# Optimization experiments

Measured on AMD Instinct MI355X. Metric: run time of the kernel, lower is better.

Reference implementation:

```python
import jax, jax.numpy as jnp
import numpy as np

NUM_FEATURES = 128
NUM_FILTERS = 128

def setup_inputs() -> dict:
    key = jax.random.key(0)
    k1, k2, k3, k4, k5 = jax.random.split(key, 5)
    B, N, F = 4, 2048, NUM_FEATURES
    x = jax.random.normal(k1, (B, N, F), dtype=jnp.float32)
    A = jax.random.normal(k2, (B, N, N), dtype=jnp.float32)
    # Conv1D(num_filters, kernel_size=1, use_bias=False) == per-node linear F -> filters
    W = jax.random.normal(k3, (F, NUM_FILTERS), dtype=jnp.float32) * (1.0 / np.sqrt(F))
    # self.a: Conv1D(1, kernel_size=1) with bias == linear filters -> 1 (shared for x_i and x_j)
    a_w = jax.random.normal(k4, (NUM_FILTERS, 1), dtype=jnp.float32) * (1.0 / np.sqrt(NUM_FILTERS))
    a_b = jax.random.normal(k5, (1,), dtype=jnp.float32) * 0.01
    bias = jnp.zeros((NUM_FILTERS,), dtype=jnp.float32)
    return {"x": x, "A": A, "W": W, "a_w": a_w, "a_b": a_b, "bias": bias}

def reference(x, A, W, a_w, a_b, bias):
    # project features: [B,N,F] @ [F,Ff] -> [B,N,Ff]
    h = jnp.einsum('bnf,fg->bng', x, W)
    # shared attention projection (x_i and x_j use the same layer): [B,N,1]
    s = jnp.einsum('bng,go->bno', h, a_w) + a_b
    # additive scores s_i + s_j^T -> [B,N,N]
    e = s + jnp.swapaxes(s, 1, 2)
    e = jnp.where(e >= 0, e, 0.2 * e)  # LeakyReLU(0.2)
    attn = jax.nn.softmax(e + A, axis=-1)
    out = jnp.einsum('bij,bjg->big', attn, h) + bias
    return out
```

## Files before the change

### kernel.cpp

```cpp
#include <hip/hip_runtime.h>
#include <hip/hip_bf16.h>
#include <stdint.h>

#define BB 4
#define NN 2048
#define FF 128

typedef __attribute__((ext_vector_type(8))) short bf16x8;
typedef __attribute__((ext_vector_type(4))) float f32x4;

__device__ inline unsigned pk_bf16(float a, float b) {
    union { float f; unsigned u; } x, y;
    x.f = a; y.f = b;
    unsigned xu = x.u + (0x7fffu + ((x.u >> 16) & 1u));
    unsigned yu = y.u + (0x7fffu + ((y.u >> 16) & 1u));
    return (xu >> 16) | (yu & 0xffff0000u);
}

#define XT_P 136
#define WT_P 136

__global__ __launch_bounds__(256) void k1_proj(
    const float* __restrict__ x, const float* __restrict__ W,
    const float* __restrict__ a_w, const float* __restrict__ a_b,
    uint16_t* __restrict__ Ht, float* __restrict__ s_out)
{
    __shared__ uint16_t xt[16 * XT_P];
    __shared__ uint16_t Wt[128 * WT_P];
    __shared__ float sredw[4 * 16];

    const int t = threadIdx.x;
    const int w = t >> 6, l = t & 63;
    const int m16 = l & 15, q = l >> 4;
    const int b = blockIdx.x >> 7;
    const int n0 = (blockIdx.x & 127) << 4;

    const int c4 = (t & 31) * 4, kh = (t >> 5) * 16;
    float4 wr0[8], wr1[8];
    #pragma unroll
    for (int kk = 0; kk < 8; ++kk) {
        const int k = kh + 2 * kk;
        wr0[kk] = *(const float4*)(W + (size_t)k * 128 + c4);
        wr1[kk] = *(const float4*)(W + (size_t)(k + 1) * 128 + c4);
    }
    {
        const int row = t >> 4, c0 = (t & 15) * 8;
        const float* xr = x + ((size_t)(b * NN + n0 + row)) * FF + c0;
        const float4 v0 = *(const float4*)xr;
        const float4 v1 = *(const float4*)(xr + 4);
        unsigned* dst = (unsigned*)(xt + row * XT_P + c0);
        dst[0] = pk_bf16(v0.x, v0.y); dst[1] = pk_bf16(v0.z, v0.w);
        dst[2] = pk_bf16(v1.x, v1.y); dst[3] = pk_bf16(v1.z, v1.w);
    }
    #pragma unroll
    for (int kk = 0; kk < 8; ++kk) {
        const int k = kh + 2 * kk;
        *(unsigned*)(Wt + (c4 + 0) * WT_P + k) = pk_bf16(wr0[kk].x, wr1[kk].x);
        *(unsigned*)(Wt + (c4 + 1) * WT_P + k) = pk_bf16(wr0[kk].y, wr1[kk].y);
        *(unsigned*)(Wt + (c4 + 2) * WT_P + k) = pk_bf16(wr0[kk].z, wr1[kk].z);
        *(unsigned*)(Wt + (c4 + 3) * WT_P + k) = pk_bf16(wr0[kk].w, wr1[kk].w);
    }
    const int g0 = (2 * w) * 16 + m16, g1 = (2 * w + 1) * 16 + m16;
    const float aw0 = a_w[g0], aw1 = a_w[g1];
    __syncthreads();

    f32x4 acc0 = {}, acc1 = {};
    bf16x8 af[4];
    #pragma unroll
    for (int dk = 0; dk < 4; ++dk)
        af[dk] = *(const bf16x8*)(xt + m16 * XT_P + dk * 32 + q * 8);
    #pragma unroll
    for (int dk = 0; dk < 4; ++dk) {
        bf16x8 b0 = *(const bf16x8*)(Wt + g0 * WT_P + dk * 32 + q * 8);
        bf16x8 b1 = *(const bf16x8*)(Wt + g1 * WT_P + dk * 32 + q * 8);
        acc0 = __builtin_amdgcn_mfma_f32_16x16x32_bf16(af[dk], b0, acc0, 0, 0, 0);
        acc1 = __builtin_amdgcn_mfma_f32_16x16x32_bf16(af[dk], b1, acc1, 0, 0, 0);
    }

    float sp[4];
    #pragma unroll
    for (int r = 0; r < 4; ++r) sp[r] = acc0[r] * aw0 + acc1[r] * aw1;
    #pragma unroll
    for (int off = 1; off < 16; off <<= 1)
        #pragma unroll
        for (int r = 0; r < 4; ++r) sp[r] += __shfl_xor(sp[r], off, 64);
    if (m16 == 0) {
        #pragma unroll
        for (int r = 0; r < 4; ++r) sredw[w * 16 + q * 4 + r] = sp[r];
    }
    {
        uint2 o0 = { pk_bf16(acc0[0], acc0[1]), pk_bf16(acc0[2], acc0[3]) };
        uint2 o1 = { pk_bf16(acc1[0], acc1[1]), pk_bf16(acc1[2], acc1[3]) };
        *(uint2*)(Ht + ((size_t)(b * 128 + g0)) * NN + n0 + q * 4) = o0;
        *(uint2*)(Ht + ((size_t)(b * 128 + g1)) * NN + n0 + q * 4) = o1;
    }
    __syncthreads();
    if (t < 16)
        s_out[b * NN + n0 + t] = sredw[t] + sredw[16 + t] + sredw[32 + t] + sredw[48 + t] + a_b[0];
}

#define JS 8
#define IRND 8

__global__ __launch_bounds__(512, 3) void k2_attn(
    const float* __restrict__ A, const uint16_t* __restrict__ Ht,
    const float* __restrict__ s, uint16_t* __restrict__ po,
    float* __restrict__ prs)
{
    __shared__ float Opw[8][16 * 68];
    __shared__ float rsw[4][16];

    const int t = threadIdx.x;
    const int w = t >> 6, l = t & 63;
    const int m16 = l & 15, q = l >> 4;
    const int gh = w & 1, jh = w >> 1;

    const int bx = blockIdx.x;
    const int js = bx & 7;
    const int is = (bx >> 3) & 15;
    const int b  = bx >> 7;
    const int j0 = js * 256;
    const int ibase = is * 128;

    const float* sb = s + b * NN;
    const float* Ab = A + (size_t)b * NN * NN;
    const uint16_t* Hb = Ht + (size_t)b * FF * NN;

    const int jcb = j0 + jh * 64;
    const int jq0 = jcb + q * 8;
    const int jq1 = jcb + 32 + q * 8;

    float4 sj0 = *(const float4*)(sb + jq0);
    float4 sj1 = *(const float4*)(sb + jq0 + 4);
    float4 sj2 = *(const float4*)(sb + jq1);
    float4 sj3 = *(const float4*)(sb + jq1 + 4);

    bf16x8 hf[4][2];
    #pragma unroll
    for (int gt = 0; gt < 4; ++gt) {
        const uint16_t* hp = Hb + (size_t)(gh * 64 + gt * 16 + m16) * NN;
        hf[gt][0] = *(const bf16x8*)(hp + jq0);
        hf[gt][1] = *(const bf16x8*)(hp + jq1);
    }

    const float* Ar = Ab + (size_t)(ibase + m16) * NN;
    float4 a0 = *(const float4*)(Ar + jq0);
    float4 a1 = *(const float4*)(Ar + jq0 + 4);
    float4 a2 = *(const float4*)(Ar + jq1);
    float4 a3 = *(const float4*)(Ar + jq1 + 4);
    float si = sb[ibase + m16];

    const size_t slice = (size_t)(js * BB + b);

    for (int r = 0; r < IRND; ++r) {
        const int i0r = ibase + r * 16;
        const int i0n = ibase + ((r + 1) & (IRND - 1)) * 16;

        const float* An = Ab + (size_t)(i0n + m16) * NN;
        float4 n0 = *(const float4*)(An + jq0);
        float4 n1 = *(const float4*)(An + jq0 + 4);
        float4 n2 = *(const float4*)(An + jq1);
        float4 n3 = *(const float4*)(An + jq1 + 4);
        const float sin_ = sb[i0n + m16];

        const float svv[16] = {sj0.x,sj0.y,sj0.z,sj0.w, sj1.x,sj1.y,sj1.z,sj1.w,
                               sj2.x,sj2.y,sj2.z,sj2.w, sj3.x,sj3.y,sj3.z,sj3.w};
        const float avv[16] = {a0.x,a0.y,a0.z,a0.w, a1.x,a1.y,a1.z,a1.w,
                               a2.x,a2.y,a2.z,a2.w, a3.x,a3.y,a3.z,a3.w};
        float pv[16]; float rs = 0.f;
        #pragma unroll
        for (int j = 0; j < 16; ++j) {
            float e = si + svv[j];
            e = fmaxf(e, 0.2f * e);
            pv[j] = __expf(e + avv[j]);
            rs += pv[j];
        }
        union { unsigned u[4]; bf16x8 v; } fa0, fa1;
        #pragma unroll
        for (int j = 0; j < 4; ++j) {
            fa0.u[j] = pk_bf16(pv[2 * j], pv[2 * j + 1]);
            fa1.u[j] = pk_bf16(pv[8 + 2 * j], pv[9 + 2 * j]);
        }

        f32x4 acc[4];
        #pragma unroll
        for (int gt = 0; gt < 4; ++gt) {
            f32x4 z = {0.f, 0.f, 0.f, 0.f};
            z = __builtin_amdgcn_mfma_f32_16x16x32_bf16(fa0.v, hf[gt][0], z, 0, 0, 0);
            acc[gt] = __builtin_amdgcn_mfma_f32_16x16x32_bf16(fa1.v, hf[gt][1], z, 0, 0, 0);
        }

        rs += __shfl_xor(rs, 16, 64);
        rs += __shfl_xor(rs, 32, 64);
        if (gh == 0 && q == 0) rsw[jh][m16] = rs;

        #pragma unroll
        for (int gt = 0; gt < 4; ++gt)
            #pragma unroll
            for (int rr = 0; rr < 4; ++rr)
                Opw[w][(q * 4 + rr) * 68 + gt * 16 + m16] = acc[gt][rr];
        asm volatile("s_waitcnt lgkmcnt(0)\n\ts_barrier" ::: "memory");

        {
            const int row = t >> 5;
            const int c4 = (t & 31) * 4;
            const int gh2 = c4 >> 6;
            const int cc = c4 & 63;
            float4 v = {0.f, 0.f, 0.f, 0.f};
            #pragma unroll
            for (int jh2 = 0; jh2 < 4; ++jh2) {
                float4 u = *(const float4*)&Opw[jh2 * 2 + gh2][row * 68 + cc];
                v.x += u.x; v.y += u.y; v.z += u.z; v.w += u.w;
            }
            unsigned* op = (unsigned*)(po + ((slice * NN + i0r + row) * FF + c4));
            op[0] = pk_bf16(v.x, v.y);
            op[1] = pk_bf16(v.z, v.w);
            if (t < 16)
                prs[slice * NN + i0r + t] = rsw[0][t] + rsw[1][t] + rsw[2][t] + rsw[3][t];
        }
        asm volatile("s_waitcnt lgkmcnt(0)\n\ts_barrier" ::: "memory");

        a0 = n0; a1 = n1; a2 = n2; a3 = n3; si = sin_;
    }
}

__global__ __launch_bounds__(256) void k3_red(
    const uint16_t* __restrict__ po, const float* __restrict__ prs,
    const float* __restrict__ bias, float* __restrict__ out)
{
    const int idx = blockIdx.x * 256 + threadIdx.x;
    const int g4 = (idx & 31) * 4;
    const int i = (idx >> 5) & (NN - 1);
    const int b = idx >> 16;

    float v0 = 0.f, v1 = 0.f, v2 = 0.f, v3 = 0.f, rsum = 0.f;
    #pragma unroll
    for (int js = 0; js < JS; ++js) {
        const size_t base = (size_t)(js * BB + b) * NN + i;
        uint2 u = *(const uint2*)(po + base * FF + g4);
        union { unsigned u; float f; } c0, c1, c2, c3;
        c0.u = u.x << 16; c1.u = u.x & 0xffff0000u;
        c2.u = u.y << 16; c3.u = u.y & 0xffff0000u;
        v0 += c0.f; v1 += c1.f; v2 += c2.f; v3 += c3.f;
        rsum += prs[base];
    }
    const float inv = 1.0f / rsum;
    float4 bv = *(const float4*)(bias + g4);
    float4 o = { v0 * inv + bv.x, v1 * inv + bv.y, v2 * inv + bv.z, v3 * inv + bv.w };
    *(float4*)(out + ((size_t)b * NN + i) * FF + g4) = o;
}

extern "C" void kernel_launch(void* const* d_in, const int* in_sizes, int n_in,
                              void* d_out, int out_size, void* d_ws, size_t ws_size,
                              hipStream_t stream) {
    const float* x    = (const float*)d_in[0];
    const float* A    = (const float*)d_in[1];
    const float* W    = (const float*)d_in[2];
    const float* a_w  = (const float*)d_in[3];
    const float* a_b  = (const float*)d_in[4];
    const float* bias = (const float*)d_in[5];
    float* out = (float*)d_out;

    char* ws = (char*)d_ws;
    uint16_t* Ht = (uint16_t*)ws;
    float* s = (float*)(ws + 2 * 1024 * 1024);
    uint16_t* po = (uint16_t*)(ws + 2 * 1024 * 1024 + 65536);
    float* prs = (float*)(ws + 2 * 1024 * 1024 + 65536 + (size_t)JS * BB * NN * FF * 2);

    k1_proj<<<BB * (NN / 16), 256, 0, stream>>>(x, W, a_w, a_b, Ht, s);
    k2_attn<<<JS * 16 * BB, 512, 0, stream>>>(A, Ht, s, po, prs);
    k3_red<<<(BB * NN * 32) / 256, 256, 0, stream>>>(po, prs, bias, out);
}
```

Baseline: 128.5 us.

## Fuse projection, attention and reduction into one cooperative kernel with grid syncs

Replaces the three separate launches with a single cooperative kernel of 256 blocks that runs projection, attention and the final reduction as phases separated by grid-wide syncs. Block work is re-partitioned so each block handles 32 nodes in projection and 256 query rows in attention, with a two-deep prefetch of A rows. Shared memory is a union of the phase layouts. This removes inter-kernel launch gaps and tail effects but adds grid barrier cost, reduces the number of blocks in the attention phase, and lowers occupancy to two blocks per CU.

```diff
diff --git a/kernel.cpp b/kernel.cpp
--- a/kernel.cpp
+++ b/kernel.cpp
@@ -1,10 +1,14 @@
 #include <hip/hip_runtime.h>
 #include <hip/hip_bf16.h>
+#include <hip/hip_cooperative_groups.h>
 #include <stdint.h>
+
+namespace cg = cooperative_groups;
 
 #define BB 4
 #define NN 2048
 #define FF 128
+#define JS 8
 
 typedef __attribute__((ext_vector_type(8))) short bf16x8;
 typedef __attribute__((ext_vector_type(4))) float f32x4;
@@ -20,234 +24,249 @@
 #define XT_P 136
 #define WT_P 136
 
-__global__ __launch_bounds__(256) void k1_proj(
-    const float* __restrict__ x, const float* __restrict__ W,
-    const float* __restrict__ a_w, const float* __restrict__ a_b,
-    uint16_t* __restrict__ Ht, float* __restrict__ s_out)
+struct SmemP1 {
+    uint16_t xt[32 * XT_P];
+    uint16_t Wt[128 * WT_P];
+    float sredw[2][64];
+};
+struct SmemP2 {
+    float Opw[8][16 * 68];
+    float rsw[4][16];
+};
+union Smem { SmemP1 p1; SmemP2 p2; };
+
+__global__ __launch_bounds__(512, 2) void fused_gat(
+    const float* __restrict__ x, const float* __restrict__ A,
+    const float* __restrict__ W, const float* __restrict__ a_w,
+    const float* __restrict__ a_b, const float* __restrict__ bias,
+    uint16_t* __restrict__ Ht, float* __restrict__ s,
+    uint16_t* __restrict__ po, float* __restrict__ prs,
+    float* __restrict__ out)
 {
-    __shared__ uint16_t xt[16 * XT_P];
-    __shared__ uint16_t Wt[128 * WT_P];
-    __shared__ float sredw[4 * 16];
+    __shared__ Smem sm;
+    cg::grid_group grid = cg::this_grid();
 
     const int t = threadIdx.x;
     const int w = t >> 6, l = t & 63;
     const int m16 = l & 15, q = l >> 4;
-    const int b = blockIdx.x >> 7;
-    const int n0 = (blockIdx.x & 127) << 4;
-
-    const int c4 = (t & 31) * 4, kh = (t >> 5) * 16;
-    float4 wr0[8], wr1[8];
-    #pragma unroll
-    for (int kk = 0; kk < 8; ++kk) {
-        const int k = kh + 2 * kk;
-        wr0[kk] = *(const float4*)(W + (size_t)k * 128 + c4);
-        wr1[kk] = *(const float4*)(W + (size_t)(k + 1) * 128 + c4);
-    }
+    const int bx = blockIdx.x;
+
     {
-        const int row = t >> 4, c0 = (t & 15) * 8;
-        const float* xr = x + ((size_t)(b * NN + n0 + row)) * FF + c0;
+        const int b = bx >> 6;
+        const int n0 = (bx & 63) << 5;
+
+        const int c4 = (t & 31) * 4, kseg = (t >> 5) * 8;
+        float4 wr[8];
+        #pragma unroll
+        for (int kk = 0; kk < 8; ++kk)
+            wr[kk] = *(const float4*)(W + (size_t)(kseg + kk) * 128 + c4);
+
+        const int xrow = t >> 4, xc0 = (t & 15) * 8;
+        const float* xr = x + ((size_t)(b * NN + n0 + xrow)) * FF + xc0;
         const float4 v0 = *(const float4*)xr;
         const float4 v1 = *(const float4*)(xr + 4);
-        unsigned* dst = (unsigned*)(xt + row * XT_P + c0);
-        dst[0] = pk_bf16(v0.x, v0.y); dst[1] = pk_bf16(v0.z, v0.w);
-        dst[2] = pk_bf16(v1.x, v1.y); dst[3] = pk_bf16(v1.z, v1.w);
+        {
+            unsigned* dst = (unsigned*)(sm.p1.xt + xrow * XT_P + xc0);
+            dst[0] = pk_bf16(v0.x, v0.y); dst[1] = pk_bf16(v0.z, v0.w);
+            dst[2] = pk_bf16(v1.x, v1.y); dst[3] = pk_bf16(v1.z, v1.w);
+        }
+        #pragma unroll
+        for (int i = 0; i < 4; ++i) {
+            unsigned* wd = (unsigned*)(sm.p1.Wt + (c4 + i) * WT_P + kseg);
+            wd[0] = pk_bf16(((const float*)&wr[0])[i], ((const float*)&wr[1])[i]);
+            wd[1] = pk_bf16(((const float*)&wr[2])[i], ((const float*)&wr[3])[i]);
+            wd[2] = pk_bf16(((const float*)&wr[4])[i], ((const float*)&wr[5])[i]);
+            wd[3] = pk_bf16(((const float*)&wr[6])[i], ((const float*)&wr[7])[i]);
+        }
+        const int rg = w >> 2, ws2 = w & 3;
+        const int g0 = (2 * ws2) * 16 + m16, g1 = (2 * ws2 + 1) * 16 + m16;
+        const float aw0 = a_w[g0], aw1 = a_w[g1];
+        __syncthreads();
+
+        f32x4 acc0 = {}, acc1 = {};
+        #pragma unroll
+        for (int dk = 0; dk < 4; ++dk) {
+            bf16x8 af = *(const bf16x8*)(sm.p1.xt + (rg * 16 + m16) * XT_P + dk * 32 + q * 8);
+            bf16x8 b0 = *(const bf16x8*)(sm.p1.Wt + g0 * WT_P + dk * 32 + q * 8);
+            bf16x8 b1 = *(const bf16x8*)(sm.p1.Wt + g1 * WT_P + dk * 32 + q * 8);
+            acc0 = __builtin_amdgcn_mfma_f32_16x16x32_bf16(af, b0, acc0, 0, 0, 0);
+            acc1 = __builtin_amdgcn_mfma_f32_16x16x32_bf16(af, b1, acc1, 0, 0, 0);
+        }
+        float sp[4];
+        #pragma unroll
+        for (int r = 0; r < 4; ++r) sp[r] = acc0[r] * aw0 + acc1[r] * aw1;
+        #pragma unroll
+        for (int off = 1; off < 16; off <<= 1)
+            #pragma unroll
+            for (int r = 0; r < 4; ++r) sp[r] += __shfl_xor(sp[r], off, 64);
+        if (m16 == 0) {
+            #pragma unroll
+            for (int r = 0; r < 4; ++r) sm.p1.sredw[rg][ws2 * 16 + q * 4 + r] = sp[r];
+        }
+        {
+            uint2 o0 = { pk_bf16(acc0[0], acc0[1]), pk_bf16(acc0[2], acc0[3]) };
+            uint2 o1 = { pk_bf16(acc1[0], acc1[1]), pk_bf16(acc1[2], acc1[3]) };
+            const int nb = n0 + rg * 16 + q * 4;
+            *(uint2*)(Ht + ((size_t)(b * FF + g0)) * NN + nb) = o0;
+            *(uint2*)(Ht + ((size_t)(b * FF + g1)) * NN + nb) = o1;
+        }
+        __syncthreads();
+        if (t < 32) {
+            const int rg2 = t >> 4, row = t & 15;
+            s[b * NN + n0 + rg2 * 16 + row] =
+                sm.p1.sredw[rg2][row] + sm.p1.sredw[rg2][16 + row] +
+                sm.p1.sredw[rg2][32 + row] + sm.p1.sredw[rg2][48 + row] + a_b[0];
+        }
     }
-    #pragma unroll
-    for (int kk = 0; kk < 8; ++kk) {
-        const int k = kh + 2 * kk;
-        *(unsigned*)(Wt + (c4 + 0) * WT_P + k) = pk_bf16(wr0[kk].x, wr1[kk].x);
-        *(unsigned*)(Wt + (c4 + 1) * WT_P + k) = pk_bf16(wr0[kk].y, wr1[kk].y);
-        *(unsigned*)(Wt + (c4 + 2) * WT_P + k) = pk_bf16(wr0[kk].z, wr1[kk].z);
-        *(unsigned*)(Wt + (c4 + 3) * WT_P + k) = pk_bf16(wr0[kk].w, wr1[kk].w);
+
+    __threadfence();
+    grid.sync();
+
+    {
+        const int gh = w & 1, jh = w >> 1;
+        const int js = bx & 7;
+        const int is = (bx >> 3) & 7;
+        const int b  = bx >> 6;
+        const int j0 = js * 256;
+        const int ibase = is * 256;
+
+        const float* sb = s + b * NN;
+        const float* Ab = A + (size_t)b * NN * NN;
+        const uint16_t* Hb = Ht + (size_t)b * FF * NN;
+
+        const int jcb = j0 + jh * 64;
+        const int jq0 = jcb + q * 8;
+        const int jq1 = jcb + 32 + q * 8;
+
+        float4 sj0 = *(const float4*)(sb + jq0);
+        float4 sj1 = *(const float4*)(sb + jq0 + 4);
+        float4 sj2 = *(const float4*)(sb + jq1);
+        float4 sj3 = *(const float4*)(sb + jq1 + 4);
+
+        bf16x8 hf[4][2];
+        #pragma unroll
+        for (int gt = 0; gt < 4; ++gt) {
+            const uint16_t* hp = Hb + (size_t)(gh * 64 + gt * 16 + m16) * NN;
+            hf[gt][0] = *(const bf16x8*)(hp + jq0);
+            hf[gt][1] = *(const bf16x8*)(hp + jq1);
+        }
+
+        const float* ArP = Ab + (size_t)(ibase + m16) * NN;
+        float4 p0 = *(const float4*)(ArP + jq0);
+        float4 p1 = *(const float4*)(ArP + jq0 + 4);
+        float4 p2 = *(const float4*)(ArP + jq1);
+        float4 p3 = *(const float4*)(ArP + jq1 + 4);
+        float siP = sb[ibase + m16];
+        const float* ArQ = Ab + (size_t)(ibase + 16 + m16) * NN;
+        float4 q0 = *(const float4*)(ArQ + jq0);
+        float4 q1 = *(const float4*)(ArQ + jq0 + 4);
+        float4 q2 = *(const float4*)(ArQ + jq1);
+        float4 q3 = *(const float4*)(ArQ + jq1 + 4);
+        float siQ = sb[ibase + 16 + m16];
+
+        const size_t slice = (size_t)(js * BB + b);
+
+        for (int r = 0; r < 16; ++r) {
+            const int i0r = ibase + r * 16;
+            const int i0n = ibase + ((r + 2) & 15) * 16;
+
+            const float* An = Ab + (size_t)(i0n + m16) * NN;
+            float4 n0_ = *(const float4*)(An + jq0);
+            float4 n1_ = *(const float4*)(An + jq0 + 4);
+            float4 n2_ = *(const float4*)(An + jq1);
+            float4 n3_ = *(const float4*)(An + jq1 + 4);
+            const float siN = sb[i0n + m16];
+
+            const float svv[16] = {sj0.x,sj0.y,sj0.z,sj0.w, sj1.x,sj1.y,sj1.z,sj1.w,
+                                   sj2.x,sj2.y,sj2.z,sj2.w, sj3.x,sj3.y,sj3.z,sj3.w};
+            const float avv[16] = {p0.x,p0.y,p0.z,p0.w, p1.x,p1.y,p1.z,p1.w,
+                                   p2.x,p2.y,p2.z,p2.w, p3.x,p3.y,p3.z,p3.w};
+            float pv[16]; float rs = 0.f;
+            #pragma unroll
+            for (int j = 0; j < 16; ++j) {
+                float e = siP + svv[j];
+                e = fmaxf(e, 0.2f * e);
+                pv[j] = __expf(e + avv[j]);
+                rs += pv[j];
+            }
+            union { unsigned u[4]; bf16x8 v; } fa0, fa1;
+            #pragma unroll
+            for (int j = 0; j < 4; ++j) {
+                fa0.u[j] = pk_bf16(pv[2 * j], pv[2 * j + 1]);
+                fa1.u[j] = pk_bf16(pv[8 + 2 * j], pv[9 + 2 * j]);
+            }
+
+            f32x4 acc[4];
+            #pragma unroll
+            for (int gt = 0; gt < 4; ++gt) {
+                f32x4 z = {0.f, 0.f, 0.f, 0.f};
+                z = __builtin_amdgcn_mfma_f32_16x16x32_bf16(fa0.v, hf[gt][0], z, 0, 0, 0);
+                acc[gt] = __builtin_amdgcn_mfma_f32_16x16x32_bf16(fa1.v, hf[gt][1], z, 0, 0, 0);
+            }
+
+            rs += __shfl_xor(rs, 16, 64);
+            rs += __shfl_xor(rs, 32, 64);
+            if (gh == 0 && q == 0) sm.p2.rsw[jh][m16] = rs;
+
+            #pragma unroll
+            for (int gt = 0; gt < 4; ++gt)
+                #pragma unroll
+                for (int rr = 0; rr < 4; ++rr)
+                    sm.p2.Opw[w][(q * 4 + rr) * 68 + gt * 16 + m16] = acc[gt][rr];
+            asm volatile("s_waitcnt lgkmcnt(0)\n\ts_barrier" ::: "memory");
+
+            {
+                const int row = t >> 5;
+                const int c4p = (t & 31) * 4;
+                const int gh2 = c4p >> 6;
+                const int cc = c4p & 63;
+                float4 v = {0.f, 0.f, 0.f, 0.f};
+                #pragma unroll
+                for (int jh2 = 0; jh2 < 4; ++jh2) {
+                    float4 u = *(const float4*)&sm.p2.Opw[jh2 * 2 + gh2][row * 68 + cc];
+                    v.x += u.x; v.y += u.y; v.z += u.z; v.w += u.w;
+                }
+                unsigned* op = (unsigned*)(po + ((slice * NN + i0r + row) * FF + c4p));
+                op[0] = pk_bf16(v.x, v.y);
+                op[1] = pk_bf16(v.z, v.w);
+                if (t < 16)
+                    prs[slice * NN + i0r + t] = sm.p2.rsw[0][t] + sm.p2.rsw[1][t] +
+                                                sm.p2.rsw[2][t] + sm.p2.rsw[3][t];
+            }
+            asm volatile("s_waitcnt lgkmcnt(0)\n\ts_barrier" ::: "memory");
+
+            p0 = q0; p1 = q1; p2 = q2; p3 = q3; siP = siQ;
+            q0 = n0_; q1 = n1_; q2 = n2_; q3 = n3_; siQ = siN;
+        }
     }
-    const int g0 = (2 * w) * 16 + m16, g1 = (2 * w + 1) * 16 + m16;
-    const float aw0 = a_w[g0], aw1 = a_w[g1];
-    __syncthreads();
-
-    f32x4 acc0 = {}, acc1 = {};
-    bf16x8 af[4];
-    #pragma unroll
-    for (int dk = 0; dk < 4; ++dk)
-        af[dk] = *(const bf16x8*)(xt + m16 * XT_P + dk * 32 + q * 8);
-    #pragma unroll
-    for (int dk = 0; dk < 4; ++dk) {
-        bf16x8 b0 = *(const bf16x8*)(Wt + g0 * WT_P + dk * 32 + q * 8);
-        bf16x8 b1 = *(const bf16x8*)(Wt + g1 * WT_P + dk * 32 + q * 8);
-        acc0 = __builtin_amdgcn_mfma_f32_16x16x32_bf16(af[dk], b0, acc0, 0, 0, 0);
-        acc1 = __builtin_amdgcn_mfma_f32_16x16x32_bf16(af[dk], b1, acc1, 0, 0, 0);
+
+    __threadfence();
+    grid.sync();
+
+    {
+        #pragma unroll
+        for (int it = 0; it < 2; ++it) {
+            const int idx = it * 131072 + bx * 512 + t;
+            const int g4 = (idx & 31) * 4;
+            const int i = (idx >> 5) & (NN - 1);
+            const int b = idx >> 16;
+            float v0 = 0.f, v1 = 0.f, v2 = 0.f, v3 = 0.f, rsum = 0.f;
+            #pragma unroll
+            for (int js2 = 0; js2 < JS; ++js2) {
+                const size_t base = (size_t)(js2 * BB + b) * NN + i;
+                uint2 u = *(const uint2*)(po + base * FF + g4);
+                union { unsigned u; float f; } c0, c1, c2, c3;
+                c0.u = u.x << 16; c1.u = u.x & 0xffff0000u;
+                c2.u = u.y << 16; c3.u = u.y & 0xffff0000u;
+                v0 += c0.f; v1 += c1.f; v2 += c2.f; v3 += c3.f;
+                rsum += prs[base];
+            }
+            const float inv = 1.0f / rsum;
+            float4 bv = *(const float4*)(bias + g4);
+            float4 o = { v0 * inv + bv.x, v1 * inv + bv.y, v2 * inv + bv.z, v3 * inv + bv.w };
+            *(float4*)(out + ((size_t)b * NN + i) * FF + g4) = o;
+        }
     }
-
-    float sp[4];
-    #pragma unroll
-    for (int r = 0; r < 4; ++r) sp[r] = acc0[r] * aw0 + acc1[r] * aw1;
-    #pragma unroll
-    for (int off = 1; off < 16; off <<= 1)
-        #pragma unroll
-        for (int r = 0; r < 4; ++r) sp[r] += __shfl_xor(sp[r], off, 64);
-    if (m16 == 0) {
-        #pragma unroll
-        for (int r = 0; r < 4; ++r) sredw[w * 16 + q * 4 + r] = sp[r];
-    }
-    {
-        uint2 o0 = { pk_bf16(acc0[0], acc0[1]), pk_bf16(acc0[2], acc0[3]) };
-        uint2 o1 = { pk_bf16(acc1[0], acc1[1]), pk_bf16(acc1[2], acc1[3]) };
-        *(uint2*)(Ht + ((size_t)(b * 128 + g0)) * NN + n0 + q * 4) = o0;
-        *(uint2*)(Ht + ((size_t)(b * 128 + g1)) * NN + n0 + q * 4) = o1;
-    }
-    __syncthreads();
-    if (t < 16)
-        s_out[b * NN + n0 + t] = sredw[t] + sredw[16 + t] + sredw[32 + t] + sredw[48 + t] + a_b[0];
-}
-
-#define JS 8
-#define IRND 8
-
-__global__ __launch_bounds__(512, 3) void k2_attn(
-    const float* __restrict__ A, const uint16_t* __restrict__ Ht,
-    const float* __restrict__ s, uint16_t* __restrict__ po,
-    float* __restrict__ prs)
-{
-    __shared__ float Opw[8][16 * 68];
-    __shared__ float rsw[4][16];
-
-    const int t = threadIdx.x;
-    const int w = t >> 6, l = t & 63;
-    const int m16 = l & 15, q = l >> 4;
-    const int gh = w & 1, jh = w >> 1;
-
-    const int bx = blockIdx.x;
-    const int js = bx & 7;
-    const int is = (bx >> 3) & 15;
-    const int b  = bx >> 7;
-    const int j0 = js * 256;
-    const int ibase = is * 128;
-
-    const float* sb = s + b * NN;
-    const float* Ab = A + (size_t)b * NN * NN;
-    const uint16_t* Hb = Ht + (size_t)b * FF * NN;
-
-    const int jcb = j0 + jh * 64;
-    const int jq0 = jcb + q * 8;
-    const int jq1 = jcb + 32 + q * 8;
-
-    float4 sj0 = *(const float4*)(sb + jq0);
-    float4 sj1 = *(const float4*)(sb + jq0 + 4);
-    float4 sj2 = *(const float4*)(sb + jq1);
-    float4 sj3 = *(const float4*)(sb + jq1 + 4);
-
-    bf16x8 hf[4][2];
-    #pragma unroll
-    for (int gt = 0; gt < 4; ++gt) {
-        const uint16_t* hp = Hb + (size_t)(gh * 64 + gt * 16 + m16) * NN;
-        hf[gt][0] = *(const bf16x8*)(hp + jq0);
-        hf[gt][1] = *(const bf16x8*)(hp + jq1);
-    }
-
-    const float* Ar = Ab + (size_t)(ibase + m16) * NN;
-    float4 a0 = *(const float4*)(Ar + jq0);
-    float4 a1 = *(const float4*)(Ar + jq0 + 4);
-    float4 a2 = *(const float4*)(Ar + jq1);
-    float4 a3 = *(const float4*)(Ar + jq1 + 4);
-    float si = sb[ibase + m16];
-
-    const size_t slice = (size_t)(js * BB + b);
-
-    for (int r = 0; r < IRND; ++r) {
-        const int i0r = ibase + r * 16;
-        const int i0n = ibase + ((r + 1) & (IRND - 1)) * 16;
-
-        const float* An = Ab + (size_t)(i0n + m16) * NN;
-        float4 n0 = *(const float4*)(An + jq0);
-        float4 n1 = *(const float4*)(An + jq0 + 4);
-        float4 n2 = *(const float4*)(An + jq1);
-        float4 n3 = *(const float4*)(An + jq1 + 4);
-        const float sin_ = sb[i0n + m16];
-
-        const float svv[16] = {sj0.x,sj0.y,sj0.z,sj0.w, sj1.x,sj1.y,sj1.z,sj1.w,
-                               sj2.x,sj2.y,sj2.z,sj2.w, sj3.x,sj3.y,sj3.z,sj3.w};
-        const float avv[16] = {a0.x,a0.y,a0.z,a0.w, a1.x,a1.y,a1.z,a1.w,
-                               a2.x,a2.y,a2.z,a2.w, a3.x,a3.y,a3.z,a3.w};
-        float pv[16]; float rs = 0.f;
-        #pragma unroll
-        for (int j = 0; j < 16; ++j) {
-            float e = si + svv[j];
-            e = fmaxf(e, 0.2f * e);
-            pv[j] = __expf(e + avv[j]);
-            rs += pv[j];
-        }
-        union { unsigned u[4]; bf16x8 v; } fa0, fa1;
-        #pragma unroll
-        for (int j = 0; j < 4; ++j) {
-            fa0.u[j] = pk_bf16(pv[2 * j], pv[2 * j + 1]);
-            fa1.u[j] = pk_bf16(pv[8 + 2 * j], pv[9 + 2 * j]);
-        }
-
-        f32x4 acc[4];
-        #pragma unroll
-        for (int gt = 0; gt < 4; ++gt) {
-            f32x4 z = {0.f, 0.f, 0.f, 0.f};
-            z = __builtin_amdgcn_mfma_f32_16x16x32_bf16(fa0.v, hf[gt][0], z, 0, 0, 0);
-            acc[gt] = __builtin_amdgcn_mfma_f32_16x16x32_bf16(fa1.v, hf[gt][1], z, 0, 0, 0);
-        }
-
-        rs += __shfl_xor(rs, 16, 64);
-        rs += __shfl_xor(rs, 32, 64);
-        if (gh == 0 && q == 0) rsw[jh][m16] = rs;
-
-        #pragma unroll
-        for (int gt = 0; gt < 4; ++gt)
-            #pragma unroll
-            for (int rr = 0; rr < 4; ++rr)
-                Opw[w][(q * 4 + rr) * 68 + gt * 16 + m16] = acc[gt][rr];
-        asm volatile("s_waitcnt lgkmcnt(0)\n\ts_barrier" ::: "memory");
-
-        {
-            const int row = t >> 5;
-            const int c4 = (t & 31) * 4;
-            const int gh2 = c4 >> 6;
-            const int cc = c4 & 63;
-            float4 v = {0.f, 0.f, 0.f, 0.f};
-            #pragma unroll
-            for (int jh2 = 0; jh2 < 4; ++jh2) {
-                float4 u = *(const float4*)&Opw[jh2 * 2 + gh2][row * 68 + cc];
-                v.x += u.x; v.y += u.y; v.z += u.z; v.w += u.w;
-            }
-            unsigned* op = (unsigned*)(po + ((slice * NN + i0r + row) * FF + c4));
-            op[0] = pk_bf16(v.x, v.y);
-            op[1] = pk_bf16(v.z, v.w);
-            if (t < 16)
-                prs[slice * NN + i0r + t] = rsw[0][t] + rsw[1][t] + rsw[2][t] + rsw[3][t];
-        }
-        asm volatile("s_waitcnt lgkmcnt(0)\n\ts_barrier" ::: "memory");
-
-        a0 = n0; a1 = n1; a2 = n2; a3 = n3; si = sin_;
-    }
-}
-
-__global__ __launch_bounds__(256) void k3_red(
-    const uint16_t* __restrict__ po, const float* __restrict__ prs,
-    const float* __restrict__ bias, float* __restrict__ out)
-{
-    const int idx = blockIdx.x * 256 + threadIdx.x;
-    const int g4 = (idx & 31) * 4;
-    const int i = (idx >> 5) & (NN - 1);
-    const int b = idx >> 16;
-
-    float v0 = 0.f, v1 = 0.f, v2 = 0.f, v3 = 0.f, rsum = 0.f;
-    #pragma unroll
-    for (int js = 0; js < JS; ++js) {
-        const size_t base = (size_t)(js * BB + b) * NN + i;
-        uint2 u = *(const uint2*)(po + base * FF + g4);
-        union { unsigned u; float f; } c0, c1, c2, c3;
-        c0.u = u.x << 16; c1.u = u.x & 0xffff0000u;
-        c2.u = u.y << 16; c3.u = u.y & 0xffff0000u;
-        v0 += c0.f; v1 += c1.f; v2 += c2.f; v3 += c3.f;
-        rsum += prs[base];
-    }
-    const float inv = 1.0f / rsum;
-    float4 bv = *(const float4*)(bias + g4);
-    float4 o = { v0 * inv + bv.x, v1 * inv + bv.y, v2 * inv + bv.z, v3 * inv + bv.w };
-    *(float4*)(out + ((size_t)b * NN + i) * FF + g4) = o;
 }
 
 extern "C" void kernel_launch(void* const* d_in, const int* in_sizes, int n_in,
@@ -267,7 +286,8 @@
     uint16_t* po = (uint16_t*)(ws + 2 * 1024 * 1024 + 65536);
     float* prs = (float*)(ws + 2 * 1024 * 1024 + 65536 + (size_t)JS * BB * NN * FF * 2);
 
-    k1_proj<<<BB * (NN / 16), 256, 0, stream>>>(x, W, a_w, a_b, Ht, s);
-    k2_attn<<<JS * 16 * BB, 512, 0, stream>>>(A, Ht, s, po, prs);
-    k3_red<<<(BB * NN * 32) / 256, 256, 0, stream>>>(po, prs, bias, out);
+    void* args[] = { (void*)&x, (void*)&A, (void*)&W, (void*)&a_w, (void*)&a_b,
+                     (void*)&bias, (void*)&Ht, (void*)&s, (void*)&po, (void*)&prs,
+                     (void*)&out };
+    hipLaunchCooperativeKernel((void*)fused_gat, dim3(256), dim3(512), args, 0, stream);
 }
```

Result: slower. 268.3 us (+108.8%).
